# Kernel optimization log

Measured on AMD Instinct MI355X. Metric: run time of the kernel, lower is better.

## Reference

```python
import jax, jax.numpy as jnp
import numpy as np


def setup_inputs() -> dict:
    key = jax.random.key(0)
    k1, k2, k3, k4 = jax.random.split(key, 4)
    E = 1_600_000
    N = 100_000
    IN, OUT = 128, 256
    edge_index = jax.random.randint(k1, (2, E), 0, N, dtype=jnp.int32)
    time_encoding = jax.random.normal(k2, (E, IN), dtype=jnp.float32)
    # Linear(in_channels, out_channels): weight [OUT, IN], bias [OUT]
    bound = 1.0 / np.sqrt(IN)
    W = jax.random.uniform(k3, (OUT, IN), minval=-bound, maxval=bound, dtype=jnp.float32)
    b = jax.random.uniform(k4, (OUT,), minval=-bound, maxval=bound, dtype=jnp.float32)
    return {"edge_index": edge_index, "time_encoding": time_encoding,
            "num_nodes": N, "W": W, "b": b}


def reference(edge_index, time_encoding, num_nodes, W, b):
    # scatter-add per-edge time encodings into destination-node buckets
    col = edge_index[1]
    agg = jax.ops.segment_sum(time_encoding, col, num_segments=num_nodes)  # [N, IN]
    # dense projection: Linear -> x @ W.T + b
    return agg @ W.T + b  # [N, OUT]
```

## Files before the change

kernel.cpp:

```cpp
#include <hip/hip_runtime.h>
#include <hip/hip_bf16.h>

#define IN_CH 128
#define OUT_CH 256
#define BLK_SCAN 1024
#define AGG_STRIDE 132

typedef __bf16 bf16x8 __attribute__((ext_vector_type(8)));
typedef float f32x4 __attribute__((ext_vector_type(4)));

__device__ inline unsigned short f2bf(float f) {
  union { float f; unsigned int u; } v; v.f = f;
  unsigned int u = v.u;
  u += 0x7FFFu + ((u >> 16) & 1u);
  return (unsigned short)(u >> 16);
}

__device__ inline float bfhi2f(unsigned int u) {
  union { unsigned int u; float f; } v; v.u = u & 0xFFFF0000u; return v.f;
}
__device__ inline float bflo2f(unsigned int u) {
  union { unsigned int u; float f; } v; v.u = u << 16; return v.f;
}

__global__ void initB_kernel(const float* __restrict__ W, unsigned short* __restrict__ Bpack,
                             int* __restrict__ cnt, int nzero) {
  int i = blockIdx.x * blockDim.x + threadIdx.x;
  if (i < nzero) cnt[i] = 0;
  if (i < IN_CH * OUT_CH) {
    const int j  = i & 7;
    const int c  = (i >> 3) & 15;
    const int kb = (i >> 7) & 3;
    const int ks = (i >> 9) & 3;
    const int tn = i >> 11;
    Bpack[i] = f2bf(W[(size_t)(tn * 16 + c) * IN_CH + ks * 32 + kb * 8 + j]);
  }
}

__global__ void hist_kernel(const int* __restrict__ col, int E, int* __restrict__ count) {
  int i = blockIdx.x * blockDim.x + threadIdx.x;
  int b = i * 4;
  if (b + 4 <= E) {
    const int4 c = *(const int4*)(col + b);
    atomicAdd(&count[c.x], 1);
    atomicAdd(&count[c.y], 1);
    atomicAdd(&count[c.z], 1);
    atomicAdd(&count[c.w], 1);
  } else {
    for (int j = b; j < E; ++j) atomicAdd(&count[col[j]], 1);
  }
}

__global__ __launch_bounds__(BLK_SCAN) void scan_block_kernel(
    const int* __restrict__ count, int N, int* __restrict__ excl, int* __restrict__ bsum) {
  __shared__ int wsum[16];
  const int tid = threadIdx.x;
  const int i = blockIdx.x * BLK_SCAN + tid;
  const int v = (i < N) ? count[i] : 0;
  int x = v;
#pragma unroll
  for (int d = 1; d < 64; d <<= 1) {
    int t = __shfl_up(x, d, 64);
    if ((tid & 63) >= d) x += t;
  }
  if ((tid & 63) == 63) wsum[tid >> 6] = x;
  __syncthreads();
  if (tid < 16) {
    int s = wsum[tid];
#pragma unroll
    for (int d = 1; d < 16; d <<= 1) {
      int t = __shfl_up(s, d, 16);
      if (tid >= d) s += t;
    }
    wsum[tid] = s;
  }
  __syncthreads();
  const int w = tid >> 6;
  const int prefix = (w == 0) ? 0 : wsum[w - 1];
  if (i < N) excl[i] = prefix + x - v;
  if (tid == BLK_SCAN - 1) bsum[blockIdx.x] = prefix + x;
}

__global__ void scan_bsum_kernel(int* __restrict__ bsum, int nb) {
  __shared__ int tmp[256];
  const int tid = threadIdx.x;
  int run = 0;
  for (int s = 0; s < nb; s += 256) {
    int v = (s + tid < nb) ? bsum[s + tid] : 0;
    tmp[tid] = v;
    __syncthreads();
    for (int d = 1; d < 256; d <<= 1) {
      int t = (tid >= d) ? tmp[tid - d] : 0;
      __syncthreads();
      tmp[tid] += t;
      __syncthreads();
    }
    if (s + tid < nb) bsum[s + tid] = run + tmp[tid] - v;
    run += tmp[255];
    __syncthreads();
  }
}

__global__ void add_offsets_kernel(int* __restrict__ excl, const int* __restrict__ bsum,
                                   int* __restrict__ cursor, int N) {
  int i = blockIdx.x * blockDim.x + threadIdx.x;
  if (i < N) {
    int o = excl[i] + bsum[i / BLK_SCAN];
    excl[i] = o;
    cursor[i] = o;
  }
}

__global__ __launch_bounds__(256) void bin_kernel(
    const float* __restrict__ te, const int* __restrict__ col,
    int* __restrict__ cursor, unsigned int* __restrict__ binned, int E) {
  const int lane = threadIdx.x & 63;
  const int gw = (blockIdx.x * 256 + threadIdx.x) >> 6;
  const int nw = (gridDim.x * 256) >> 6;
  for (int base = gw * 4; base < E; base += nw * 4) {
    int ne = E - base; if (ne > 4) ne = 4;
    int mypos = 0;
    if (lane < ne) {
      const int c = col[base + lane];
      mypos = atomicAdd(&cursor[c], 1);
    }
#pragma unroll
    for (int j = 0; j < 4; ++j) {
      if (j < ne) {
        const int pos = __builtin_amdgcn_readlane(mypos, j);
        const float lo = te[(size_t)(base + j) * IN_CH + lane];
        const float hi = te[(size_t)(base + j) * IN_CH + lane + 64];
        binned[(size_t)pos * 64 + lane] =
            (unsigned int)f2bf(lo) | ((unsigned int)f2bf(hi) << 16);
      }
    }
  }
}

__global__ __launch_bounds__(256) void phase2_kernel(
    const unsigned int* __restrict__ binned, const int* __restrict__ start,
    const int* __restrict__ cend, const unsigned short* __restrict__ Bpack,
    const float* __restrict__ bias, float* __restrict__ out, int N) {
  __shared__ float agg[16][AGG_STRIDE];
  const int tid = threadIdx.x;
  const int wave = tid >> 6;
  const int lane = tid & 63;
  const int half = lane >> 5;
  const int li   = lane & 31;
  const int m0 = blockIdx.x * 16;

#pragma unroll
  for (int q = 0; q < 4; ++q) {
    const int g = wave * 4 + q;
    const int n = m0 + g;
    float s00 = 0.f, s01 = 0.f, s10 = 0.f, s11 = 0.f;
    if (n < N) {
      const int s0 = start[n];
      const int e0 = cend[n];
      for (int r0 = s0; r0 < e0; r0 += 16) {
        const int rem = e0 - r0;
        uint2 v[8];
#pragma unroll
        for (int j = 0; j < 8; ++j) {
          int row = r0 + 2 * j + half;
          row = (row < e0) ? row : (e0 - 1);
          v[j] = *(const uint2*)(binned + (size_t)row * 64 + li * 2);
        }
#pragma unroll
        for (int j = 0; j < 8; ++j) {
          const float c = (2 * j + half < rem) ? 1.f : 0.f;
          s00 = fmaf(c, bflo2f(v[j].x), s00);
          s01 = fmaf(c, bfhi2f(v[j].x), s01);
          s10 = fmaf(c, bflo2f(v[j].y), s10);
          s11 = fmaf(c, bfhi2f(v[j].y), s11);
        }
      }
    }
    s00 += __shfl_down(s00, 32);
    s01 += __shfl_down(s01, 32);
    s10 += __shfl_down(s10, 32);
    s11 += __shfl_down(s11, 32);
    if (half == 0) {
      *(float2*)(&agg[g][2 * li])      = make_float2(s00, s10);
      *(float2*)(&agg[g][2 * li + 64]) = make_float2(s01, s11);
    }
  }
  __syncthreads();

  const int r  = lane & 15;
  const int kb = lane >> 4;

  bf16x8 a[4];
#pragma unroll
  for (int ks = 0; ks < 4; ++ks) {
    bf16x8 t;
#pragma unroll
    for (int j = 0; j < 8; ++j) t[j] = (__bf16)agg[r][ks * 32 + kb * 8 + j];
    a[ks] = t;
  }

  f32x4 acc[4];
#pragma unroll
  for (int ct = 0; ct < 4; ++ct) acc[ct] = (f32x4){0.f, 0.f, 0.f, 0.f};

#pragma unroll
  for (int ct = 0; ct < 4; ++ct) {
    const int tn = wave * 4 + ct;
#pragma unroll
    for (int ks = 0; ks < 4; ++ks) {
      const bf16x8 bb = *(const bf16x8*)(Bpack + (size_t)((((tn * 4 + ks) * 4 + kb) * 16 + r) * 8));
      acc[ct] = __builtin_amdgcn_mfma_f32_16x16x32_bf16(a[ks], bb, acc[ct], 0, 0, 0);
    }
  }

#pragma unroll
  for (int ct = 0; ct < 4; ++ct) {
    const int colo = wave * 64 + ct * 16 + r;
    const float bv = bias[colo];
#pragma unroll
    for (int j = 0; j < 4; ++j) {
      const int m = m0 + kb * 4 + j;
      if (m < N) out[(size_t)m * OUT_CH + colo] = acc[ct][j] + bv;
    }
  }
}

extern "C" void kernel_launch(void* const* d_in, const int* in_sizes, int n_in,
                              void* d_out, int out_size, void* d_ws, size_t ws_size,
                              hipStream_t stream) {
  const int* edge_index = (const int*)d_in[0];
  const float* te       = (const float*)d_in[1];
  const float* W        = (const float*)d_in[3];
  const float* bias     = (const float*)d_in[4];
  float* out            = (float*)d_out;

  const int E = in_sizes[0] / 2;
  const int N = out_size / OUT_CH;
  const int* col = edge_index + E;

  const int Np = (N + 3) & ~3;

  char* p = (char*)d_ws;
  unsigned short* Bpack = (unsigned short*)p;      p += 65536;
  int* cnt    = (int*)p;                           p += (size_t)Np * 4;
  int* start  = (int*)p;                           p += (size_t)Np * 4;
  int* cursor = (int*)p;                           p += (size_t)Np * 4;
  int* bsum   = (int*)p;                           p += 4096 * 4;
  p = (char*)(((uintptr_t)p + 255) & ~(uintptr_t)255);
  unsigned int* binned = (unsigned int*)p;

  const int nb = (N + BLK_SCAN - 1) / BLK_SCAN;
  const int init_n = (N > IN_CH * OUT_CH) ? N : IN_CH * OUT_CH;
  const int K = (N + 15) / 16;

  hipLaunchKernelGGL(initB_kernel, dim3((init_n + 255) / 256), dim3(256), 0, stream,
                     W, Bpack, cnt, N);
  hipLaunchKernelGGL(hist_kernel, dim3((E / 4 + 255) / 256), dim3(256), 0, stream,
                     col, E, cnt);
  hipLaunchKernelGGL(scan_block_kernel, dim3(nb), dim3(BLK_SCAN), 0, stream,
                     cnt, N, start, bsum);
  hipLaunchKernelGGL(scan_bsum_kernel, dim3(1), dim3(256), 0, stream, bsum, nb);
  hipLaunchKernelGGL(add_offsets_kernel, dim3((N + 255) / 256), dim3(256), 0, stream,
                     start, bsum, cursor, N);
  hipLaunchKernelGGL(bin_kernel, dim3(2048), dim3(256), 0, stream,
                     te, col, cursor, binned, E);
  hipLaunchKernelGGL(phase2_kernel, dim3(K), dim3(256), 0, stream,
                     binned, start, cursor, Bpack, bias, out, N);
}
```

Before: 463.5 us.

## Batch first-chunk gathers across nodes and widen edge binning loads

The binning kernel now handles 8 edges per wave iteration and reads each edge row with a contiguous float2 load, which changes the packing to adjacent channel pairs. The aggregation kernel issues the first 16-row gather for all four nodes of a wave before reducing any of them, raising memory-level parallelism on the irregular binned reads. It then stores the reduced sums as float4 to match the new packing. The cost is more registers held at once (32 uint2 values per lane), which may lower occupancy.

Measured after the change: 453.6 us, median of 2. 1.02x faster.

```diff
diff --git a/kernel.cpp b/kernel.cpp
--- a/kernel.cpp
+++ b/kernel.cpp
@@ -117,21 +117,19 @@
   const int lane = threadIdx.x & 63;
   const int gw = (blockIdx.x * 256 + threadIdx.x) >> 6;
   const int nw = (gridDim.x * 256) >> 6;
-  for (int base = gw * 4; base < E; base += nw * 4) {
-    int ne = E - base; if (ne > 4) ne = 4;
+  for (int base = gw * 8; base < E; base += nw * 8) {
+    int ne = E - base; if (ne > 8) ne = 8;
     int mypos = 0;
     if (lane < ne) {
-      const int c = col[base + lane];
-      mypos = atomicAdd(&cursor[c], 1);
-    }
-#pragma unroll
-    for (int j = 0; j < 4; ++j) {
+      mypos = atomicAdd(&cursor[col[base + lane]], 1);
+    }
+#pragma unroll
+    for (int j = 0; j < 8; ++j) {
       if (j < ne) {
         const int pos = __builtin_amdgcn_readlane(mypos, j);
-        const float lo = te[(size_t)(base + j) * IN_CH + lane];
-        const float hi = te[(size_t)(base + j) * IN_CH + lane + 64];
+        const float2 v = *(const float2*)(te + (size_t)(base + j) * IN_CH + lane * 2);
         binned[(size_t)pos * 64 + lane] =
-            (unsigned int)f2bf(lo) | ((unsigned int)f2bf(hi) << 16);
+            (unsigned int)f2bf(v.x) | ((unsigned int)f2bf(v.y) << 16);
       }
     }
   }
@@ -149,40 +147,62 @@
   const int li   = lane & 31;
   const int m0 = blockIdx.x * 16;
 
+  int s0[4], e0[4];
+  float acc[4][4];
+  uint2 v[4][8];
 #pragma unroll
   for (int q = 0; q < 4; ++q) {
-    const int g = wave * 4 + q;
-    const int n = m0 + g;
-    float s00 = 0.f, s01 = 0.f, s10 = 0.f, s11 = 0.f;
-    if (n < N) {
-      const int s0 = start[n];
-      const int e0 = cend[n];
-      for (int r0 = s0; r0 < e0; r0 += 16) {
-        const int rem = e0 - r0;
-        uint2 v[8];
-#pragma unroll
-        for (int j = 0; j < 8; ++j) {
-          int row = r0 + 2 * j + half;
-          row = (row < e0) ? row : (e0 - 1);
-          v[j] = *(const uint2*)(binned + (size_t)row * 64 + li * 2);
-        }
-#pragma unroll
-        for (int j = 0; j < 8; ++j) {
-          const float c = (2 * j + half < rem) ? 1.f : 0.f;
-          s00 = fmaf(c, bflo2f(v[j].x), s00);
-          s01 = fmaf(c, bfhi2f(v[j].x), s01);
-          s10 = fmaf(c, bflo2f(v[j].y), s10);
-          s11 = fmaf(c, bfhi2f(v[j].y), s11);
-        }
+    const int n = m0 + wave * 4 + q;
+    s0[q] = (n < N) ? start[n] : 0;
+    e0[q] = (n < N) ? cend[n] : 0;
+#pragma unroll
+    for (int c = 0; c < 4; ++c) acc[q][c] = 0.f;
+  }
+#pragma unroll
+  for (int q = 0; q < 4; ++q) {
+#pragma unroll
+    for (int j = 0; j < 8; ++j) {
+      int row = s0[q] + 2 * j + half;
+      row = (row < e0[q]) ? row : (e0[q] > s0[q] ? e0[q] - 1 : 0);
+      v[q][j] = *(const uint2*)(binned + (size_t)row * 64 + li * 2);
+    }
+  }
+#pragma unroll
+  for (int q = 0; q < 4; ++q) {
+    const int rem = e0[q] - s0[q];
+#pragma unroll
+    for (int j = 0; j < 8; ++j) {
+      const float c = (2 * j + half < rem) ? 1.f : 0.f;
+      acc[q][0] = fmaf(c, bflo2f(v[q][j].x), acc[q][0]);
+      acc[q][1] = fmaf(c, bfhi2f(v[q][j].x), acc[q][1]);
+      acc[q][2] = fmaf(c, bflo2f(v[q][j].y), acc[q][2]);
+      acc[q][3] = fmaf(c, bfhi2f(v[q][j].y), acc[q][3]);
+    }
+    for (int r0 = s0[q] + 16; r0 < e0[q]; r0 += 16) {
+      const int rem2 = e0[q] - r0;
+      uint2 w[8];
+#pragma unroll
+      for (int j = 0; j < 8; ++j) {
+        int row = r0 + 2 * j + half;
+        row = (row < e0[q]) ? row : (e0[q] - 1);
+        w[j] = *(const uint2*)(binned + (size_t)row * 64 + li * 2);
       }
-    }
-    s00 += __shfl_down(s00, 32);
-    s01 += __shfl_down(s01, 32);
-    s10 += __shfl_down(s10, 32);
-    s11 += __shfl_down(s11, 32);
+#pragma unroll
+      for (int j = 0; j < 8; ++j) {
+        const float c = (2 * j + half < rem2) ? 1.f : 0.f;
+        acc[q][0] = fmaf(c, bflo2f(w[j].x), acc[q][0]);
+        acc[q][1] = fmaf(c, bfhi2f(w[j].x), acc[q][1]);
+        acc[q][2] = fmaf(c, bflo2f(w[j].y), acc[q][2]);
+        acc[q][3] = fmaf(c, bfhi2f(w[j].y), acc[q][3]);
+      }
+    }
+    acc[q][0] += __shfl_down(acc[q][0], 32);
+    acc[q][1] += __shfl_down(acc[q][1], 32);
+    acc[q][2] += __shfl_down(acc[q][2], 32);
+    acc[q][3] += __shfl_down(acc[q][3], 32);
     if (half == 0) {
-      *(float2*)(&agg[g][2 * li])      = make_float2(s00, s10);
-      *(float2*)(&agg[g][2 * li + 64]) = make_float2(s01, s11);
+      *(float4*)(&agg[wave * 4 + q][4 * li]) =
+          make_float4(acc[q][0], acc[q][1], acc[q][2], acc[q][3]);
     }
   }
   __syncthreads();
@@ -199,9 +219,9 @@
     a[ks] = t;
   }
 
-  f32x4 acc[4];
-#pragma unroll
-  for (int ct = 0; ct < 4; ++ct) acc[ct] = (f32x4){0.f, 0.f, 0.f, 0.f};
+  f32x4 accm[4];
+#pragma unroll
+  for (int ct = 0; ct < 4; ++ct) accm[ct] = (f32x4){0.f, 0.f, 0.f, 0.f};
 
 #pragma unroll
   for (int ct = 0; ct < 4; ++ct) {
@@ -209,7 +229,7 @@
 #pragma unroll
     for (int ks = 0; ks < 4; ++ks) {
       const bf16x8 bb = *(const bf16x8*)(Bpack + (size_t)((((tn * 4 + ks) * 4 + kb) * 16 + r) * 8));
-      acc[ct] = __builtin_amdgcn_mfma_f32_16x16x32_bf16(a[ks], bb, acc[ct], 0, 0, 0);
+      accm[ct] = __builtin_amdgcn_mfma_f32_16x16x32_bf16(a[ks], bb, accm[ct], 0, 0, 0);
     }
   }
 
@@ -220,7 +240,7 @@
 #pragma unroll
     for (int j = 0; j < 4; ++j) {
       const int m = m0 + kb * 4 + j;
-      if (m < N) out[(size_t)m * OUT_CH + colo] = acc[ct][j] + bv;
+      if (m < N) out[(size_t)m * OUT_CH + colo] = accm[ct][j] + bv;
     }
   }
 }
```
